# Kernel optimization log

Hardware: AMD Instinct MI355X
Metric: run time of the kernel (lower is better)

The kernel has to match this reference:

```python
import jax, jax.numpy as jnp
import numpy as np

PC_RANGE = np.asarray([-51.2, -51.2, -5.0, 51.2, 51.2, 3.0], dtype=np.float32)
DIMS = PC_RANGE[3:] - PC_RANGE[:3]
H, W = 256, 256
B, M, D = 4, 100, 128
EFF_MIN, EFF_MAX = 1.0, 6.0


def setup_inputs() -> dict:
    key = jax.random.key(0)
    k1, k2, k3 = jax.random.split(key, 3)
    atten_map = jax.random.uniform(k1, (B, H * W, D), dtype=jnp.float32)
    u = jax.random.uniform(k2, (B, M, 7), dtype=jnp.float32)
    xy = u[..., :2] * 92.16 - 46.08
    z = u[..., 2:3] * 8.0 - 5.0
    lw = u[..., 3:5] * 4.0 + 1.0             # box l, w in [1, 5] m
    hgt = u[..., 5:6] * 3.0 + 1.0
    yaw = u[..., 6:7] * (2.0 * np.pi) - np.pi
    gt_bboxes = jnp.concatenate([xy, z, lw, hgt, yaw], axis=-1)
    gt_labels = jax.random.randint(k3, (B, M), 0, 10)
    return {"atten_map": atten_map, "gt_bboxes": gt_bboxes, "gt_labels": gt_labels}


def _grid_centers():
    # matches np.meshgrid(range(w), range(h)) -> flat index g: col = g % W, row = g // W
    gx = jnp.tile((jnp.arange(W, dtype=jnp.float32) + 0.5) / W * DIMS[0] + PC_RANGE[0], H)
    gy = jnp.repeat((jnp.arange(H, dtype=jnp.float32) + 0.5) / H * DIMS[1] + PC_RANGE[1], W)
    return jnp.stack([gx, gy], axis=1)  # [HW, 2]


def _center_to_corner_2d(centers, dims, angles):
    # second.pytorch corner ordering and rotation convention
    corners_norm = jnp.asarray([[-0.5, -0.5], [-0.5, 0.5], [0.5, 0.5], [0.5, -0.5]], dtype=jnp.float32)
    corners = dims[:, None, :] * corners_norm  # [M, 4, 2]
    c, s = jnp.cos(angles)[:, None], jnp.sin(angles)[:, None]
    rx = corners[..., 0] * c + corners[..., 1] * s
    ry = -corners[..., 0] * s + corners[..., 1] * c
    return jnp.stack([rx, ry], axis=-1) + centers[:, None, :]  # [M, 4, 2]


def _forward(atten_map, gt_bboxes):
    grids = _grid_centers()  # [HW, 2]
    hw = H * W

    def per_scene(atten, boxes):
        centers = boxes[:, :2]
        lw = boxes[:, 3:5]
        ratio_l = jnp.clip(DIMS[0] / W / lw[:, 0], EFF_MIN, EFF_MAX)
        ratio_w = jnp.clip(DIMS[1] / H / lw[:, 1], EFF_MIN, EFF_MAX)
        eff_dims = jnp.stack([lw[:, 0] * ratio_l, lw[:, 1] * ratio_w], axis=1)
        corners = _center_to_corner_2d(centers, eff_dims, boxes[:, -1])  # [M, 4, 2]
        edges = jnp.roll(corners, -1, axis=1) - corners                  # [M, 4, 2]
        dx = grids[None, None, :, 0] - corners[:, :, None, 0]            # [M, 4, HW]
        dy = grids[None, None, :, 1] - corners[:, :, None, 1]
        cross = edges[:, :, None, 0] * dy - edges[:, :, None, 1] * dx    # [M, 4, HW]
        inside = jnp.all(cross >= 0, axis=1) | jnp.all(cross <= 0, axis=1)  # [M, HW]
        # force-include the grid nearest to each GT center
        d2 = jnp.sum((grids[None] - centers[:, None]) ** 2, axis=-1)     # [M, HW]
        nearest = jnp.arange(hw)[None, :] == jnp.argmin(d2, axis=1)[:, None]
        pos = inside | nearest                                           # [M, HW]

        # sequential per-box flag assignment with overlap-kill semantics:
        # grids already owned by an earlier box are reset to -1, fresh grids get i
        def body(flag, xi):
            pos_i, i = xi
            flag = jnp.where(pos_i, jnp.where(flag == -1, i, -1), flag)
            return flag, None

        flag, _ = jax.lax.scan(body, -jnp.ones(hw, jnp.int32),
                               (pos, jnp.arange(M, dtype=jnp.int32)))

        v = jnp.var(atten, axis=1, ddof=1)  # per-grid unbiased variance over D, [HW]
        seg = jnp.where(flag >= 0, flag, M)
        sums = jax.ops.segment_sum(v, seg, num_segments=M + 1)[:M]
        cnts = jax.ops.segment_sum(jnp.ones(hw, jnp.float32), seg, num_segments=M + 1)[:M]
        valid = cnts > 0
        box_mean = sums / jnp.maximum(cnts, 1.0)
        loss = -jnp.sum(jnp.where(valid, box_mean, 0.0))
        return loss, jnp.sum(valid.astype(jnp.float32))

    losses, nums = jax.vmap(per_scene)(atten_map, gt_bboxes)
    var_loss = jnp.sum(losses)
    var_pos_num = jnp.maximum(jnp.sum(nums), 1.0)
    return var_loss / var_pos_num


def reference(atten_map, gt_bboxes, gt_labels):
    # gt_labels is accepted (signature parity) but unused by the loss, as in the original
    return _forward(atten_map, gt_bboxes)
```

## Files before the change

kernel.cpp:

```cpp
#include <hip/hip_runtime.h>

#define Bn 4
#define Mn 100
#define Dn 128

__global__ __launch_bounds__(256) void flag_kernel(
    const float* __restrict__ boxes,
    unsigned int* __restrict__ rowcnt,
    unsigned int* __restrict__ cells,
    float* __restrict__ gz)
{
    __shared__ float abox[Mn * 18];
    __shared__ int   am[Mn];
    __shared__ int   wcnt[4], wbase[4];
    __shared__ int   nactS, nflag;
    __shared__ int   clist[256];

    const int b  = blockIdx.x >> 8;
    const int y  = blockIdx.x & 255;
    const int tx = threadIdx.x;

    if (blockIdx.x < 2 * Bn * Mn && tx == 0) gz[blockIdx.x] = 0.0f;
    if (tx == 0) nflag = 0;

    const float DIMS0 = 51.2f + 51.2f;
    float gy = __fadd_rn(__fmul_rn((y + 0.5f) * (1.0f / 256.0f), DIMS0), -51.2f);

    float px[4], py[4], ex[4], ey[4];
    bool act = false;
    if (tx < Mn) {
        const float* bx = boxes + (size_t)(b * Mn + tx) * 7;
        float cx = bx[0], cy = bx[1];
        float l = bx[3], w = bx[4], yaw = bx[6];
        const float cellw = DIMS0 / 256.0f;
        float rl = fminf(fmaxf(cellw / l, 1.0f), 6.0f);
        float rw = fminf(fmaxf(cellw / w, 1.0f), 6.0f);
        float el = __fmul_rn(l, rl);
        float ew = __fmul_rn(w, rw);
        float c = cosf(yaw), s = sinf(yaw);
        const float nx[4] = {-0.5f, -0.5f, 0.5f, 0.5f};
        const float ny[4] = {-0.5f, 0.5f, 0.5f, -0.5f};
        #pragma unroll
        for (int k = 0; k < 4; k++) {
            float ox = __fmul_rn(el, nx[k]);
            float oy = __fmul_rn(ew, ny[k]);
            float rx = __fadd_rn(__fmul_rn(ox, c), __fmul_rn(oy, s));
            float ry = __fadd_rn(__fmul_rn(-ox, s), __fmul_rn(oy, c));
            px[k] = __fadd_rn(rx, cx);
            py[k] = __fadd_rn(ry, cy);
        }
        #pragma unroll
        for (int k = 0; k < 4; k++) {
            ex[k] = __fsub_rn(px[(k + 1) & 3], px[k]);
            ey[k] = __fsub_rn(py[(k + 1) & 3], py[k]);
        }
        float r = 0.5f * sqrtf(el * el + ew * ew) + 0.01f;
        act = fabsf(gy - cy) <= r;
    }

    unsigned long long mb = __ballot(act);
    int wid = tx >> 6;
    if ((tx & 63) == 0) wcnt[wid] = __popcll(mb);
    __syncthreads();
    if (tx == 0) {
        wbase[0] = 0;
        wbase[1] = wcnt[0];
        wbase[2] = wcnt[0] + wcnt[1];
        wbase[3] = wbase[2] + wcnt[2];
        nactS    = wbase[3] + wcnt[3];
    }
    __syncthreads();
    const int nact = nactS;
    if (nact == 0) {
        if (tx == 0) rowcnt[blockIdx.x] = 0;
        return;
    }
    if (act) {
        int slot = wbase[wid] + __popcll(mb & ((1ull << (tx & 63)) - 1ull));
        float* o = abox + slot * 18;
        #pragma unroll
        for (int k = 0; k < 4; k++) {
            o[k * 2] = px[k];  o[k * 2 + 1] = py[k];
            o[8 + k * 2] = ex[k]; o[8 + k * 2 + 1] = ey[k];
        }
        am[slot] = tx;
    }
    __syncthreads();

    float gx = __fadd_rn(__fmul_rn((tx + 0.5f) * (1.0f / 256.0f), DIMS0), -51.2f);
    int flag = -1;
    for (int j = 0; j < nact; j++) {
        const float* o = &abox[j * 18];
        bool ge = true, le = true;
        #pragma unroll
        for (int k = 0; k < 4; k++) {
            float dx = __fsub_rn(gx, o[k * 2]);
            float dy = __fsub_rn(gy, o[k * 2 + 1]);
            float cr = __fsub_rn(__fmul_rn(o[8 + k * 2], dy),
                                 __fmul_rn(o[8 + k * 2 + 1], dx));
            ge = ge && (cr >= 0.0f);
            le = le && (cr <= 0.0f);
        }
        if (ge || le) flag = (flag == -1) ? am[j] : -1;
    }

    if (flag >= 0) {
        int idx = atomicAdd(&nflag, 1);
        clist[idx] = (flag << 8) | tx;
    }
    __syncthreads();
    if (tx == 0) rowcnt[blockIdx.x] = nflag;
    for (int i = tx; i < nflag; i += 256)
        cells[(blockIdx.x << 8) + i] = clist[i];
}

__global__ __launch_bounds__(256) void gather_kernel(
    const float* __restrict__ atten,
    const unsigned int* __restrict__ rowcnt,
    const unsigned int* __restrict__ cells,
    float* __restrict__ gsum, float* __restrict__ gcnt)
{
    __shared__ float ssum[Mn], scnt[Mn];
    const int tx  = threadIdx.x;
    const int row = blockIdx.x >> 1;
    const int b   = row >> 8;
    const unsigned int n = rowcnt[row];

    if (tx < Mn) { ssum[tx] = 0.0f; scnt[tx] = 0.0f; }
    if (n == 0) return;
    __syncthreads();

    const int g = ((blockIdx.x & 1) << 3) + (tx >> 5);
    const int lane = tx & 31;
    const unsigned int base = (unsigned int)row << 8;
    for (unsigned int j = g; j < n; j += 16) {
        unsigned int e = cells[base + j];
        int x = e & 255, m = e >> 8;
        const float4* p = reinterpret_cast<const float4*>(
            atten + ((size_t)base + x) * Dn) + lane;
        float4 xv = *p;
        float s = xv.x + xv.y + xv.z + xv.w;
        float q = xv.x * xv.x + xv.y * xv.y + xv.z * xv.z + xv.w * xv.w;
        #pragma unroll
        for (int d = 16; d; d >>= 1) {
            s += __shfl_xor(s, d);
            q += __shfl_xor(q, d);
        }
        if (lane == 0) {
            float vv = (q - s * s * (1.0f / 128.0f)) * (1.0f / 127.0f);
            atomicAdd(&ssum[m], vv);
            atomicAdd(&scnt[m], 1.0f);
        }
    }
    __syncthreads();
    if (tx < Mn && scnt[tx] > 0.0f) {
        atomicAdd(&gsum[b * Mn + tx], ssum[tx]);
        atomicAdd(&gcnt[b * Mn + tx], scnt[tx]);
    }
}

__global__ __launch_bounds__(512) void final_kernel(const float* __restrict__ gsum,
                                                    const float* __restrict__ gcnt,
                                                    float* __restrict__ out) {
    __shared__ float sl[8], sn[8];
    int t = threadIdx.x;
    float loss = 0.0f, num = 0.0f;
    if (t < Bn * Mn) {
        float c = gcnt[t];
        if (c > 0.0f) {
            loss = -(gsum[t] / fmaxf(c, 1.0f));
            num = 1.0f;
        }
    }
    #pragma unroll
    for (int m = 32; m; m >>= 1) {
        loss += __shfl_xor(loss, m);
        num  += __shfl_xor(num, m);
    }
    if ((t & 63) == 0) { sl[t >> 6] = loss; sn[t >> 6] = num; }
    __syncthreads();
    if (t == 0) {
        float L = 0.0f, N = 0.0f;
        #pragma unroll
        for (int i = 0; i < 8; i++) { L += sl[i]; N += sn[i]; }
        out[0] = L / fmaxf(N, 1.0f);
    }
}

extern "C" void kernel_launch(void* const* d_in, const int* in_sizes, int n_in,
                              void* d_out, int out_size, void* d_ws, size_t ws_size,
                              hipStream_t stream) {
    const float* atten = (const float*)d_in[0];
    const float* boxes = (const float*)d_in[1];
    float* out = (float*)d_out;

    float* gsum = (float*)d_ws;
    float* gcnt = gsum + Bn * Mn;
    unsigned int* rowcnt = (unsigned int*)((char*)d_ws + 3200);
    unsigned int* cells  = (unsigned int*)((char*)d_ws + 8192);

    flag_kernel<<<Bn * 256, 256, 0, stream>>>(boxes, rowcnt, cells, gsum);
    gather_kernel<<<2 * Bn * 256, 256, 0, stream>>>(atten, rowcnt, cells, gsum, gcnt);
    final_kernel<<<1, 512, 0, stream>>>(gsum, gcnt, out);
}
```

Baseline: 20.49 us.

## Fuse flag and gather kernels, precompute box geometry in a prep kernel

Box corner and edge geometry is now computed once per box in a small prep kernel instead of in every row block. The flag and gather stages are merged into one kernel, so the cell list stays in shared memory and the rowcnt/cells round trip through global memory goes away. The row is split over four blocks that each redo the flag test, and each warp loads two cells per iteration to raise memory-level parallelism. The cost is that the point-in-box test is computed four times per row, and an extra small kernel launch is added.

```diff
diff --git a/kernel.cpp b/kernel.cpp
--- a/kernel.cpp
+++ b/kernel.cpp
@@ -3,61 +3,80 @@
 #define Bn 4
 #define Mn 100
 #define Dn 128
-
-__global__ __launch_bounds__(256) void flag_kernel(
+#define BS 18
+
+__global__ __launch_bounds__(256) void prep_kernel(
     const float* __restrict__ boxes,
-    unsigned int* __restrict__ rowcnt,
-    unsigned int* __restrict__ cells,
+    float* __restrict__ bws,
     float* __restrict__ gz)
 {
-    __shared__ float abox[Mn * 18];
+    const int t = blockIdx.x * 256 + threadIdx.x;
+    for (int i = t; i < 2 * Bn * Mn; i += 512) gz[i] = 0.0f;
+    if (t >= Bn * Mn) return;
+
+    const float* bx = boxes + (size_t)t * 7;
+    float cx = bx[0], cy = bx[1];
+    float l = bx[3], w = bx[4], yaw = bx[6];
+    const float DIMS0 = 51.2f + 51.2f;
+    const float cellw = DIMS0 / 256.0f;
+    float rl = fminf(fmaxf(cellw / l, 1.0f), 6.0f);
+    float rw = fminf(fmaxf(cellw / w, 1.0f), 6.0f);
+    float el = __fmul_rn(l, rl);
+    float ew = __fmul_rn(w, rw);
+    float c = cosf(yaw), s = sinf(yaw);
+    const float nx[4] = {-0.5f, -0.5f, 0.5f, 0.5f};
+    const float ny[4] = {-0.5f, 0.5f, 0.5f, -0.5f};
+    float px[4], py[4];
+    #pragma unroll
+    for (int k = 0; k < 4; k++) {
+        float ox = __fmul_rn(el, nx[k]);
+        float oy = __fmul_rn(ew, ny[k]);
+        float rx = __fadd_rn(__fmul_rn(ox, c), __fmul_rn(oy, s));
+        float ry = __fadd_rn(__fmul_rn(-ox, s), __fmul_rn(oy, c));
+        px[k] = __fadd_rn(rx, cx);
+        py[k] = __fadd_rn(ry, cy);
+    }
+    float* o = bws + (size_t)t * BS;
+    #pragma unroll
+    for (int k = 0; k < 4; k++) { o[k * 2] = px[k]; o[k * 2 + 1] = py[k]; }
+    #pragma unroll
+    for (int k = 0; k < 4; k++) {
+        o[8 + k * 2]     = __fsub_rn(px[(k + 1) & 3], px[k]);
+        o[8 + k * 2 + 1] = __fsub_rn(py[(k + 1) & 3], py[k]);
+    }
+    o[16] = cy;
+    o[17] = 0.5f * sqrtf(el * el + ew * ew) + 0.01f;
+}
+
+__global__ __launch_bounds__(256) void fused_kernel(
+    const float* __restrict__ atten,
+    const float* __restrict__ bws,
+    float* __restrict__ gsum, float* __restrict__ gcnt)
+{
+    __shared__ float sb[Mn * BS];
     __shared__ int   am[Mn];
     __shared__ int   wcnt[4], wbase[4];
     __shared__ int   nactS, nflag;
     __shared__ int   clist[256];
-
-    const int b  = blockIdx.x >> 8;
-    const int y  = blockIdx.x & 255;
-    const int tx = threadIdx.x;
-
-    if (blockIdx.x < 2 * Bn * Mn && tx == 0) gz[blockIdx.x] = 0.0f;
+    __shared__ float ssum[Mn], scnt[Mn];
+
+    const int row = blockIdx.x >> 2;
+    const int q   = blockIdx.x & 3;
+    const int b   = row >> 8;
+    const int y   = row & 255;
+    const int tx  = threadIdx.x;
+
+    for (int i = tx; i < Mn * BS; i += 256) sb[i] = bws[b * Mn * BS + i];
     if (tx == 0) nflag = 0;
+    if (tx < Mn) { ssum[tx] = 0.0f; scnt[tx] = 0.0f; }
+    __syncthreads();
 
     const float DIMS0 = 51.2f + 51.2f;
     float gy = __fadd_rn(__fmul_rn((y + 0.5f) * (1.0f / 256.0f), DIMS0), -51.2f);
 
-    float px[4], py[4], ex[4], ey[4];
     bool act = false;
-    if (tx < Mn) {
-        const float* bx = boxes + (size_t)(b * Mn + tx) * 7;
-        float cx = bx[0], cy = bx[1];
-        float l = bx[3], w = bx[4], yaw = bx[6];
-        const float cellw = DIMS0 / 256.0f;
-        float rl = fminf(fmaxf(cellw / l, 1.0f), 6.0f);
-        float rw = fminf(fmaxf(cellw / w, 1.0f), 6.0f);
-        float el = __fmul_rn(l, rl);
-        float ew = __fmul_rn(w, rw);
-        float c = cosf(yaw), s = sinf(yaw);
-        const float nx[4] = {-0.5f, -0.5f, 0.5f, 0.5f};
-        const float ny[4] = {-0.5f, 0.5f, 0.5f, -0.5f};
-        #pragma unroll
-        for (int k = 0; k < 4; k++) {
-            float ox = __fmul_rn(el, nx[k]);
-            float oy = __fmul_rn(ew, ny[k]);
-            float rx = __fadd_rn(__fmul_rn(ox, c), __fmul_rn(oy, s));
-            float ry = __fadd_rn(__fmul_rn(-ox, s), __fmul_rn(oy, c));
-            px[k] = __fadd_rn(rx, cx);
-            py[k] = __fadd_rn(ry, cy);
-        }
-        #pragma unroll
-        for (int k = 0; k < 4; k++) {
-            ex[k] = __fsub_rn(px[(k + 1) & 3], px[k]);
-            ey[k] = __fsub_rn(py[(k + 1) & 3], py[k]);
-        }
-        float r = 0.5f * sqrtf(el * el + ew * ew) + 0.01f;
-        act = fabsf(gy - cy) <= r;
-    }
-
+    if (tx < Mn)
+        act = fabsf(gy - sb[tx * BS + 16]) <= sb[tx * BS + 17];
     unsigned long long mb = __ballot(act);
     int wid = tx >> 6;
     if ((tx & 63) == 0) wcnt[wid] = __popcll(mb);
@@ -71,18 +90,9 @@
     }
     __syncthreads();
     const int nact = nactS;
-    if (nact == 0) {
-        if (tx == 0) rowcnt[blockIdx.x] = 0;
-        return;
-    }
+    if (nact == 0) return;
     if (act) {
         int slot = wbase[wid] + __popcll(mb & ((1ull << (tx & 63)) - 1ull));
-        float* o = abox + slot * 18;
-        #pragma unroll
-        for (int k = 0; k < 4; k++) {
-            o[k * 2] = px[k];  o[k * 2 + 1] = py[k];
-            o[8 + k * 2] = ex[k]; o[8 + k * 2 + 1] = ey[k];
-        }
         am[slot] = tx;
     }
     __syncthreads();
@@ -90,7 +100,8 @@
     float gx = __fadd_rn(__fmul_rn((tx + 0.5f) * (1.0f / 256.0f), DIMS0), -51.2f);
     int flag = -1;
     for (int j = 0; j < nact; j++) {
-        const float* o = &abox[j * 18];
+        const int m = am[j];
+        const float* o = &sb[m * BS];
         bool ge = true, le = true;
         #pragma unroll
         for (int k = 0; k < 4; k++) {
@@ -101,55 +112,49 @@
             ge = ge && (cr >= 0.0f);
             le = le && (cr <= 0.0f);
         }
-        if (ge || le) flag = (flag == -1) ? am[j] : -1;
-    }
-
+        if (ge || le) flag = (flag == -1) ? m : -1;
+    }
     if (flag >= 0) {
         int idx = atomicAdd(&nflag, 1);
         clist[idx] = (flag << 8) | tx;
     }
     __syncthreads();
-    if (tx == 0) rowcnt[blockIdx.x] = nflag;
-    for (int i = tx; i < nflag; i += 256)
-        cells[(blockIdx.x << 8) + i] = clist[i];
-}
-
-__global__ __launch_bounds__(256) void gather_kernel(
-    const float* __restrict__ atten,
-    const unsigned int* __restrict__ rowcnt,
-    const unsigned int* __restrict__ cells,
-    float* __restrict__ gsum, float* __restrict__ gcnt)
-{
-    __shared__ float ssum[Mn], scnt[Mn];
-    const int tx  = threadIdx.x;
-    const int row = blockIdx.x >> 1;
-    const int b   = row >> 8;
-    const unsigned int n = rowcnt[row];
-
-    if (tx < Mn) { ssum[tx] = 0.0f; scnt[tx] = 0.0f; }
-    if (n == 0) return;
-    __syncthreads();
-
-    const int g = ((blockIdx.x & 1) << 3) + (tx >> 5);
+    const int n = nflag;
+
+    const int gg   = (q << 3) + (tx >> 5);
     const int lane = tx & 31;
-    const unsigned int base = (unsigned int)row << 8;
-    for (unsigned int j = g; j < n; j += 16) {
-        unsigned int e = cells[base + j];
-        int x = e & 255, m = e >> 8;
-        const float4* p = reinterpret_cast<const float4*>(
-            atten + ((size_t)base + x) * Dn) + lane;
-        float4 xv = *p;
-        float s = xv.x + xv.y + xv.z + xv.w;
-        float q = xv.x * xv.x + xv.y * xv.y + xv.z * xv.z + xv.w * xv.w;
+    const size_t rowbase = (size_t)row << 8;
+    for (int j = gg; j < n; j += 64) {
+        int e0 = clist[j];
+        int j1 = j + 32;
+        bool h1 = j1 < n;
+        int e1 = h1 ? clist[j1] : e0;
+        const float4* p0 = reinterpret_cast<const float4*>(
+            atten + (rowbase + (e0 & 255)) * Dn) + lane;
+        const float4* p1 = reinterpret_cast<const float4*>(
+            atten + (rowbase + (e1 & 255)) * Dn) + lane;
+        float4 a0 = *p0;
+        float4 a1 = *p1;
+        float s0 = a0.x + a0.y + a0.z + a0.w;
+        float q0 = a0.x * a0.x + a0.y * a0.y + a0.z * a0.z + a0.w * a0.w;
+        float s1 = a1.x + a1.y + a1.z + a1.w;
+        float q1 = a1.x * a1.x + a1.y * a1.y + a1.z * a1.z + a1.w * a1.w;
         #pragma unroll
         for (int d = 16; d; d >>= 1) {
-            s += __shfl_xor(s, d);
-            q += __shfl_xor(q, d);
+            s0 += __shfl_xor(s0, d);
+            q0 += __shfl_xor(q0, d);
+            s1 += __shfl_xor(s1, d);
+            q1 += __shfl_xor(q1, d);
         }
         if (lane == 0) {
-            float vv = (q - s * s * (1.0f / 128.0f)) * (1.0f / 127.0f);
-            atomicAdd(&ssum[m], vv);
-            atomicAdd(&scnt[m], 1.0f);
+            float v0 = (q0 - s0 * s0 * (1.0f / 128.0f)) * (1.0f / 127.0f);
+            atomicAdd(&ssum[e0 >> 8], v0);
+            atomicAdd(&scnt[e0 >> 8], 1.0f);
+            if (h1) {
+                float v1 = (q1 - s1 * s1 * (1.0f / 128.0f)) * (1.0f / 127.0f);
+                atomicAdd(&ssum[e1 >> 8], v1);
+                atomicAdd(&scnt[e1 >> 8], 1.0f);
+            }
         }
     }
     __syncthreads();
@@ -196,10 +201,9 @@
 
     float* gsum = (float*)d_ws;
     float* gcnt = gsum + Bn * Mn;
-    unsigned int* rowcnt = (unsigned int*)((char*)d_ws + 3200);
-    unsigned int* cells  = (unsigned int*)((char*)d_ws + 8192);
-
-    flag_kernel<<<Bn * 256, 256, 0, stream>>>(boxes, rowcnt, cells, gsum);
-    gather_kernel<<<2 * Bn * 256, 256, 0, stream>>>(atten, rowcnt, cells, gsum, gcnt);
+    float* bws  = (float*)((char*)d_ws + 4096);
+
+    prep_kernel<<<2, 256, 0, stream>>>(boxes, bws, gsum);
+    fused_kernel<<<4 * Bn * 256, 256, 0, stream>>>(atten, bws, gsum, gcnt);
     final_kernel<<<1, 512, 0, stream>>>(gsum, gcnt, out);
 }
```

New measurement: 28.02 us. 36.8% more time.

## Fuse flag and gather kernels, replace global atomics with per-row partials

Applied to the files above, without the earlier changes.

Merges the flagging and variance-gather kernels into one, so each row block reads atten for its flagged cells directly from its shared cell list instead of going through a global cells buffer. Each block writes compact per-box partial sums and counts, packed as box index plus count in a float, and the final single block reduces them with shared atomics, which removes global atomics and one kernel launch. Gather loads are batched four at a time per warp to raise memory-level parallelism. The trade-offs are fewer blocks in the gather phase (1024 instead of 2048) and a heavier final kernel that scans 102400 slots in a single block.

```diff
diff --git a/kernel.cpp b/kernel.cpp
--- a/kernel.cpp
+++ b/kernel.cpp
@@ -4,24 +4,25 @@
 #define Mn 100
 #define Dn 128
 
-__global__ __launch_bounds__(256) void flag_kernel(
+__global__ __launch_bounds__(256) void fused_kernel(
+    const float* __restrict__ atten,
     const float* __restrict__ boxes,
-    unsigned int* __restrict__ rowcnt,
-    unsigned int* __restrict__ cells,
-    float* __restrict__ gz)
+    unsigned int* __restrict__ bcnt,
+    float2* __restrict__ trip)
 {
     __shared__ float abox[Mn * 18];
     __shared__ int   am[Mn];
     __shared__ int   wcnt[4], wbase[4];
-    __shared__ int   nactS, nflag;
+    __shared__ int   nactS, nflag, ntS;
     __shared__ int   clist[256];
+    __shared__ float ssum[Mn], scnt[Mn];
 
     const int b  = blockIdx.x >> 8;
     const int y  = blockIdx.x & 255;
     const int tx = threadIdx.x;
 
-    if (blockIdx.x < 2 * Bn * Mn && tx == 0) gz[blockIdx.x] = 0.0f;
-    if (tx == 0) nflag = 0;
+    if (tx == 0) { nflag = 0; ntS = 0; }
+    if (tx < Mn) { ssum[tx] = 0.0f; scnt[tx] = 0.0f; }
 
     const float DIMS0 = 51.2f + 51.2f;
     float gy = __fadd_rn(__fmul_rn((y + 0.5f) * (1.0f / 256.0f), DIMS0), -51.2f);
@@ -72,7 +73,7 @@
     __syncthreads();
     const int nact = nactS;
     if (nact == 0) {
-        if (tx == 0) rowcnt[blockIdx.x] = 0;
+        if (tx == 0) bcnt[blockIdx.x] = 0;
         return;
     }
     if (act) {
@@ -103,86 +104,108 @@
         }
         if (ge || le) flag = (flag == -1) ? am[j] : -1;
     }
-
     if (flag >= 0) {
         int idx = atomicAdd(&nflag, 1);
         clist[idx] = (flag << 8) | tx;
     }
     __syncthreads();
-    if (tx == 0) rowcnt[blockIdx.x] = nflag;
-    for (int i = tx; i < nflag; i += 256)
-        cells[(blockIdx.x << 8) + i] = clist[i];
+    const int n = nflag;
+    if (n == 0) {
+        if (tx == 0) bcnt[blockIdx.x] = 0;
+        return;
+    }
+
+    const int g = tx >> 5, lane = tx & 31;
+    const size_t rowbase = (size_t)blockIdx.x << 8;
+    for (int j0 = g; j0 < n; j0 += 32) {
+        int   e[4];
+        bool  h[4];
+        float4 a[4];
+        #pragma unroll
+        for (int u = 0; u < 4; u++) {
+            int j = j0 + u * 8;
+            h[u] = j < n;
+            e[u] = clist[h[u] ? j : j0];
+            const float4* p = reinterpret_cast<const float4*>(
+                atten + (rowbase + (e[u] & 255)) * Dn) + lane;
+            a[u] = *p;
+        }
+        #pragma unroll
+        for (int u = 0; u < 4; u++) {
+            if (!h[u]) continue;
+            float s = a[u].x + a[u].y + a[u].z + a[u].w;
+            float q = a[u].x * a[u].x + a[u].y * a[u].y
+                    + a[u].z * a[u].z + a[u].w * a[u].w;
+            #pragma unroll
+            for (int d = 16; d; d >>= 1) {
+                s += __shfl_xor(s, d);
+                q += __shfl_xor(q, d);
+            }
+            if (lane == 0) {
+                float vv = (q - s * s * (1.0f / 128.0f)) * (1.0f / 127.0f);
+                atomicAdd(&ssum[e[u] >> 8], vv);
+                atomicAdd(&scnt[e[u] >> 8], 1.0f);
+            }
+        }
+    }
+    __syncthreads();
+
+    if (tx < Mn && scnt[tx] > 0.0f) {
+        int slot = atomicAdd(&ntS, 1);
+        trip[blockIdx.x * Mn + slot] =
+            make_float2(ssum[tx], (float)(tx * 1024) + scnt[tx]);
+    }
+    __syncthreads();
+    if (tx == 0) bcnt[blockIdx.x] = (unsigned int)ntS;
 }
 
-__global__ __launch_bounds__(256) void gather_kernel(
-    const float* __restrict__ atten,
-    const unsigned int* __restrict__ rowcnt,
-    const unsigned int* __restrict__ cells,
-    float* __restrict__ gsum, float* __restrict__ gcnt)
+__global__ __launch_bounds__(1024) void final_kernel(
+    const unsigned int* __restrict__ bcnt,
+    const float2* __restrict__ trip,
+    float* __restrict__ out)
 {
-    __shared__ float ssum[Mn], scnt[Mn];
-    const int tx  = threadIdx.x;
-    const int row = blockIdx.x >> 1;
-    const int b   = row >> 8;
-    const unsigned int n = rowcnt[row];
-
-    if (tx < Mn) { ssum[tx] = 0.0f; scnt[tx] = 0.0f; }
-    if (n == 0) return;
-    __syncthreads();
-
-    const int g = ((blockIdx.x & 1) << 3) + (tx >> 5);
-    const int lane = tx & 31;
-    const unsigned int base = (unsigned int)row << 8;
-    for (unsigned int j = g; j < n; j += 16) {
-        unsigned int e = cells[base + j];
-        int x = e & 255, m = e >> 8;
-        const float4* p = reinterpret_cast<const float4*>(
-            atten + ((size_t)base + x) * Dn) + lane;
-        float4 xv = *p;
-        float s = xv.x + xv.y + xv.z + xv.w;
-        float q = xv.x * xv.x + xv.y * xv.y + xv.z * xv.z + xv.w * xv.w;
-        #pragma unroll
-        for (int d = 16; d; d >>= 1) {
-            s += __shfl_xor(s, d);
-            q += __shfl_xor(q, d);
-        }
-        if (lane == 0) {
-            float vv = (q - s * s * (1.0f / 128.0f)) * (1.0f / 127.0f);
-            atomicAdd(&ssum[m], vv);
-            atomicAdd(&scnt[m], 1.0f);
-        }
-    }
-    __syncthreads();
-    if (tx < Mn && scnt[tx] > 0.0f) {
-        atomicAdd(&gsum[b * Mn + tx], ssum[tx]);
-        atomicAdd(&gcnt[b * Mn + tx], scnt[tx]);
-    }
-}
-
-__global__ __launch_bounds__(512) void final_kernel(const float* __restrict__ gsum,
-                                                    const float* __restrict__ gcnt,
-                                                    float* __restrict__ out) {
-    __shared__ float sl[8], sn[8];
-    int t = threadIdx.x;
+    __shared__ unsigned int bc[Bn * 256];
+    __shared__ float bsum[Bn * Mn], bcn[Bn * Mn];
+    __shared__ float sl[16], sn[16];
+    const int tx = threadIdx.x;
+
+    bc[tx] = bcnt[tx];
+    for (int i = tx; i < Bn * Mn; i += 1024) { bsum[i] = 0.0f; bcn[i] = 0.0f; }
+    __syncthreads();
+
+    for (int p = tx; p < 1024 * Mn; p += 1024) {
+        int row = p / Mn;
+        int i   = p - row * Mn;
+        if (i < (int)bc[row]) {
+            float2 t = trip[p];
+            int code = (int)t.y;
+            int m    = code >> 10;
+            int bin  = (row >> 8) * Mn + m;
+            atomicAdd(&bsum[bin], t.x);
+            atomicAdd(&bcn[bin], (float)(code & 1023));
+        }
+    }
+    __syncthreads();
+
     float loss = 0.0f, num = 0.0f;
-    if (t < Bn * Mn) {
-        float c = gcnt[t];
+    if (tx < Bn * Mn) {
+        float c = bcn[tx];
         if (c > 0.0f) {
-            loss = -(gsum[t] / fmaxf(c, 1.0f));
-            num = 1.0f;
+            loss = -(bsum[tx] / fmaxf(c, 1.0f));
+            num  = 1.0f;
         }
     }
     #pragma unroll
-    for (int m = 32; m; m >>= 1) {
-        loss += __shfl_xor(loss, m);
-        num  += __shfl_xor(num, m);
-    }
-    if ((t & 63) == 0) { sl[t >> 6] = loss; sn[t >> 6] = num; }
-    __syncthreads();
-    if (t == 0) {
+    for (int d = 32; d; d >>= 1) {
+        loss += __shfl_xor(loss, d);
+        num  += __shfl_xor(num, d);
+    }
+    if ((tx & 63) == 0) { sl[tx >> 6] = loss; sn[tx >> 6] = num; }
+    __syncthreads();
+    if (tx == 0) {
         float L = 0.0f, N = 0.0f;
         #pragma unroll
-        for (int i = 0; i < 8; i++) { L += sl[i]; N += sn[i]; }
+        for (int i = 0; i < 16; i++) { L += sl[i]; N += sn[i]; }
         out[0] = L / fmaxf(N, 1.0f);
     }
 }
@@ -194,12 +217,9 @@
     const float* boxes = (const float*)d_in[1];
     float* out = (float*)d_out;
 
-    float* gsum = (float*)d_ws;
-    float* gcnt = gsum + Bn * Mn;
-    unsigned int* rowcnt = (unsigned int*)((char*)d_ws + 3200);
-    unsigned int* cells  = (unsigned int*)((char*)d_ws + 8192);
-
-    flag_kernel<<<Bn * 256, 256, 0, stream>>>(boxes, rowcnt, cells, gsum);
-    gather_kernel<<<2 * Bn * 256, 256, 0, stream>>>(atten, rowcnt, cells, gsum, gcnt);
-    final_kernel<<<1, 512, 0, stream>>>(gsum, gcnt, out);
+    unsigned int* bcnt = (unsigned int*)d_ws;
+    float2* trip = (float2*)((char*)d_ws + 4096);
+
+    fused_kernel<<<Bn * 256, 256, 0, stream>>>(atten, boxes, bcnt, trip);
+    final_kernel<<<1, 1024, 0, stream>>>(bcnt, trip, out);
 }
```

Measured after the change: 42.60 us. +107.9%, slower.
